# Optimization experiments

Measured on AMD Instinct MI355X. Metric: run time of the kernel, lower is better.

Reference implementation:

```python
import jax, jax.numpy as jnp
import numpy as np

N = 4096        # nodes == batch_size (GFN operates on dense N x N adjacency)
E = 65536       # edges per view (avg degree 16)
IN = 512        # per-view input feature dim
HV = [128, 64]  # per-view GCN dims
HM = [64, 64]   # fused-graph GCN dims
VIEWS = 3


def setup_inputs() -> dict:
    key = jax.random.key(0)
    ks = iter(jax.random.split(key, 64))

    def xavier(shape):
        lim = float(np.sqrt(6.0 / (shape[0] + shape[1])))
        return jax.random.uniform(next(ks), shape, minval=-lim, maxval=lim, dtype=jnp.float32)

    inp = {}
    for v in range(VIEWS):
        inp[f"x{v}"] = jax.random.normal(next(ks), (N, IN), dtype=jnp.float32)
        inp[f"src{v}"] = jax.random.randint(next(ks), (E,), 0, N, dtype=jnp.int32)
        inp[f"dst{v}"] = jax.random.randint(next(ks), (E,), 0, N, dtype=jnp.int32)
        inp[f"Wv{v}0"] = xavier((IN, HV[0]))
        inp[f"bv{v}0"] = jnp.zeros((HV[0],), jnp.float32)
        inp[f"Wv{v}1"] = xavier((HV[0], HV[1]))
        inp[f"bv{v}1"] = jnp.zeros((HV[1],), jnp.float32)
        inp[f"Wf{v}"] = xavier((HV[1], HV[1]))  # FeatureFusion weight
    # GFN: Linear(N -> N/2) -> ReLU -> Linear(N/2 -> N)
    inp["Wg1"] = xavier((N, N // 2)); inp["bg1"] = jnp.zeros((N // 2,), jnp.float32)
    inp["Wg2"] = xavier((N // 2, N)); inp["bg2"] = jnp.zeros((N,), jnp.float32)
    # fused-graph GCN layers
    inp["Wm0"] = xavier((HV[1], HM[0])); inp["bm0"] = jnp.zeros((HM[0],), jnp.float32)
    inp["Wm1"] = xavier((HM[0], HM[1])); inp["bm1"] = jnp.zeros((HM[1],), jnp.float32)
    return inp


def _deg_norms(src, dst):
    # DGL GraphConv norm='both': scale by out-deg(src)^-1/2 and in-deg(dst)^-1/2, degrees clamped to >=1
    ones = jnp.ones(src.shape[0], jnp.float32)
    dout = jnp.maximum(jax.ops.segment_sum(ones, src, num_segments=N), 1.0)
    din = jnp.maximum(jax.ops.segment_sum(ones, dst, num_segments=N), 1.0)
    return dout ** -0.5, din ** -0.5


def _gconv(x, W, b, src, dst, do_isqrt, di_isqrt, act):
    h = (x * do_isqrt[:, None]) @ W            # [N, out] (W commutes with row scaling)
    agg = jax.ops.segment_sum(h[src], dst, num_segments=N)
    h = agg * di_isqrt[:, None] + b
    return act(h)


def reference(x0, x1, x2, src0, dst0, src1, dst1, src2, dst2,
              Wv00, bv00, Wv01, bv01, Wv10, bv10, Wv11, bv11, Wv20, bv20, Wv21, bv21,
              Wf0, Wf1, Wf2, Wg1, bg1, Wg2, bg2, Wm0, bm0, Wm1, bm1):
    ident = lambda t: t
    xs = [x0, x1, x2]
    edges = [(src0, dst0), (src1, dst1), (src2, dst2)]
    Wv = [(Wv00, bv00, Wv01, bv01), (Wv10, bv10, Wv11, bv11), (Wv20, bv20, Wv21, bv21)]
    Wf = [Wf0, Wf1, Wf2]

    # per-view GCN stacks (relu on first layer, identity on last)
    feats = []
    for v in range(VIEWS):
        src, dst = edges[v]
        do_i, di_i = _deg_norms(src, dst)
        W0, b0, W1, b1 = Wv[v]
        f = _gconv(xs[v], W0, b0, src, dst, do_i, di_i, jax.nn.relu)
        f = _gconv(f, W1, b1, src, dst, do_i, di_i, ident)
        feats.append(f)

    # FeatureFusion (dropout omitted for determinism): sum(f @ Wf), softmax over features, relu
    z = feats[0] @ Wf[0] + feats[1] @ Wf[1] + feats[2] @ Wf[2]
    z = jax.nn.relu(jax.nn.softmax(z, axis=1))

    # consensus graph: sum of per-view dense adjacencies -> GFN -> clamp -> round(+0.1)
    adj = jnp.zeros((N, N), jnp.float32)
    for src, dst in edges:
        adj = adj + jnp.zeros((N, N), jnp.float32).at[src, dst].set(1.0)
    fused = jax.nn.relu(adj @ Wg1 + bg1) @ Wg2 + bg2
    fused = jnp.round(jnp.clip(fused, 0.0, 1.0) + 0.1)
    adj_r = fused

    # rebuild binary graph (went through numpy in original -> stop_gradient), symmetrize, add self-loops
    sym = jax.lax.stop_gradient(fused)
    sym = sym + sym.T
    A = jnp.maximum((sym > 0).astype(jnp.float32), jnp.eye(N, dtype=jnp.float32))
    deg = A.sum(axis=1)
    dn = deg ** -0.5

    # fused-graph GCN layers (dense normalized SpMM form since A is already dense)
    h = z
    h = jax.nn.relu(((A @ (h * dn[:, None])) * dn[:, None]) @ Wm0 + bm0)
    h = ((A @ (h * dn[:, None])) * dn[:, None]) @ Wm1 + bm1

    # InnerProductDecoder with identity activation; all `views` entries of adj_rec are identical
    adj_rec = h @ h.T
    return (adj_r, adj_rec, h)
```

## Files before the change

kernel.cpp:

```cpp
#include <hip/hip_runtime.h>
#include <math.h>

#define NNODES 4096
#define NEDGES 65536

typedef short bf16x8 __attribute__((ext_vector_type(8)));
typedef short short4v __attribute__((ext_vector_type(4)));
typedef float f32x4 __attribute__((ext_vector_type(4)));

struct Ptr3  { const float* p[3]; };
struct Ptr3i { const int*   p[3]; };
struct Ptr3h { const short* p[3]; };

__device__ __forceinline__ short f2bf(float f) {
    unsigned u = __builtin_bit_cast(unsigned, f);
    unsigned r = (u + 0x7FFFu + ((u >> 16) & 1u)) >> 16;
    return (short)r;
}
__device__ __forceinline__ float bf2f(short s) {
    return __builtin_bit_cast(float, ((unsigned)(unsigned short)s) << 16);
}

__device__ __forceinline__ void gload_lds16(const void* g, void* l) {
    __builtin_amdgcn_global_load_lds(
        (const __attribute__((address_space(1))) unsigned*)g,
        (__attribute__((address_space(3))) unsigned*)l, 16, 0, 0);
}

template<int ACT>
__global__ __launch_bounds__(512, 1)
void gm_k(const short* __restrict__ A, const short* __restrict__ Bt,
          const float* __restrict__ bias, void* __restrict__ Cout, void* __restrict__ Cout1,
          unsigned char* __restrict__ Pout, int M, int Nn, int K, int lda, int ldb)
{
    constexpr int SLOT = 32768;
    __shared__ short lds[2 * SLOT];
    const int tid = threadIdx.x;
    const int lane = tid & 63;
    const int wave = tid >> 6;
    const int wm = wave >> 2, wn = wave & 3;
    const int z = blockIdx.z;
    A  += (size_t)z * K;
    Bt += (size_t)z * K;
    void* Cw = (ACT == 3 && z == 1) ? Cout1 : Cout;
    const int gx = gridDim.x, nwg = gx * gridDim.y;
    int w = blockIdx.y * gx + blockIdx.x;
    const int q8 = nwg >> 3;
    w = (w & 7) * q8 + (w >> 3);
    const int bm0 = (w / gx) * 256, bn0 = (w % gx) * 256;
    const int NT = K >> 6;

    auto stageH = [&](int t, int part) {
        if (t >= NT) return;
        const int k0 = t << 6;
        char* base = (char*)(lds + (t & 1) * SLOT);
        const int isB = (part < 2);
        const int h = part & 1;
#pragma unroll
        for (int r = 0; r < 2; ++r) {
            int o = r * 8192 + tid * 16;
            int row = o >> 7;
            int grow = h * 128 + row;
            int scol = (((o >> 4) & 7) ^ (grow & 7)) << 3;
            const short* gsrc = isB ? (Bt + (size_t)(bn0 + grow) * ldb + k0 + scol)
                                    : (A  + (size_t)(bm0 + grow) * lda + k0 + scol);
            gload_lds16(gsrc, base + (isB ? 32768 : 0) + h * 16384 + r * 8192 + wave * 1024);
        }
    };

    f32x4 acc[8][4] = {};
    bf16x8 aF[4][2];
    bf16x8 bF[4][2];

#define PH(QM, QN, TCUR, T1, P1, T2, P2, VM)                                          \
    {                                                                                 \
        const short* As_ = lds + ((TCUR) & 1) * SLOT;                                 \
        const short* Bs_ = As_ + 16384;                                               \
        if constexpr ((QN) == 0) {                                                    \
            _Pragma("unroll") for (int kk = 0; kk < 2; ++kk) {                        \
                const int h_ = kk * 4 + (lane >> 4);                                  \
                _Pragma("unroll") for (int i = 0; i < 4; ++i) {                       \
                    int r_ = wm * 128 + (QM) * 64 + i * 16 + (lane & 15);             \
                    aF[i][kk] = *(const bf16x8*)(As_ + r_ * 64 + ((h_ ^ (r_ & 7)) << 3)); \
                }                                                                     \
            }                                                                         \
        }                                                                             \
        if constexpr ((QM) == 0) {                                                    \
            _Pragma("unroll") for (int kk = 0; kk < 2; ++kk) {                        \
                const int h_ = kk * 4 + (lane >> 4);                                  \
                _Pragma("unroll") for (int j = 0; j < 2; ++j) {                       \
                    int r_ = wn * 64 + ((QN) * 2 + j) * 16 + (lane & 15);             \
                    bF[(QN) * 2 + j][kk] = *(const bf16x8*)(Bs_ + r_ * 64 + ((h_ ^ (r_ & 7)) << 3)); \
                }                                                                     \
            }                                                                         \
        }                                                                             \
        if ((P1) >= 0) stageH(T1, P1);                                                \
        if ((P2) >= 0) stageH(T2, P2);                                                \
        if constexpr ((QM) == 0 && (QN) == 0) {                                       \
            asm volatile("s_waitcnt lgkmcnt(8)" ::: "memory");                        \
        }                                                                             \
        __builtin_amdgcn_s_barrier();                                                 \
        __builtin_amdgcn_s_setprio(1);                                                \
        _Pragma("unroll") for (int kk = 0; kk < 2; ++kk)                              \
            _Pragma("unroll") for (int i = 0; i < 4; ++i)                             \
                _Pragma("unroll") for (int j = 0; j < 2; ++j)                         \
                    acc[(QM) * 4 + i][(QN) * 2 + j] =                                 \
                        __builtin_amdgcn_mfma_f32_16x16x32_bf16(                      \
                            aF[i][kk], bF[(QN) * 2 + j][kk],                          \
                            acc[(QM) * 4 + i][(QN) * 2 + j], 0, 0, 0);                \
        __builtin_amdgcn_s_setprio(0);                                                \
        if ((VM) == 6)      { asm volatile("s_waitcnt vmcnt(6)" ::: "memory");        \
                              __builtin_amdgcn_sched_barrier(0); }                    \
        else if ((VM) == 0) { asm volatile("s_waitcnt vmcnt(0)" ::: "memory");        \
                              __builtin_amdgcn_sched_barrier(0); }                    \
        __builtin_amdgcn_s_barrier();                                                 \
    }

    stageH(0, 0); stageH(0, 1); stageH(0, 2); stageH(0, 3);
    if (NT > 1) { stageH(1, 0); stageH(1, 1); stageH(1, 2); }
    if (NT > 1) { asm volatile("s_waitcnt vmcnt(6)" ::: "memory"); }
    else        { asm volatile("s_waitcnt vmcnt(0)" ::: "memory"); }
    __builtin_amdgcn_sched_barrier(0);
    __builtin_amdgcn_s_barrier();

    for (int it = 0; it < NT / 2; ++it) {
        const int t0 = 2 * it, t1 = t0 + 1, t2 = t0 + 2, t3 = t0 + 3;
        const int vm4 = (t2 < NT) ? 6 : 0;
        const int vm8 = (t3 < NT) ? 6 : 0;
        PH(0, 0, t0, t1, 3,  0, -1, -1)
        PH(0, 1, t0,  0, -1, 0, -1, -1)
        PH(1, 0, t0, t2, 0, t2,  1, -1)
        PH(1, 1, t0, t2, 2,  0, -1, vm4)
        PH(0, 0, t1, t2, 3,  0, -1, -1)
        PH(0, 1, t1,  0, -1, 0, -1, -1)
        PH(1, 0, t1, t3, 0, t3,  1, -1)
        PH(1, 1, t1, t3, 2,  0, -1, vm8)
    }
    if (NT & 1) {
        const int tl = NT - 1;
        PH(0, 0, tl, 0, -1, 0, -1, -1)
        PH(0, 1, tl, 0, -1, 0, -1, -1)
        PH(1, 0, tl, 0, -1, 0, -1, -1)
        PH(1, 1, tl, 0, -1, 0, -1, -1)
    }
#undef PH

    const int cr = (lane >> 4) * 4;
    const int cc = lane & 15;
#pragma unroll
    for (int im = 0; im < 8; ++im) {
#pragma unroll
        for (int jn = 0; jn < 4; ++jn) {
            int col = bn0 + wn * 64 + jn * 16 + cc;
            float bv = bias ? bias[col] : 0.f;
#pragma unroll
            for (int q2 = 0; q2 < 4; ++q2) {
                int row = bm0 + wm * 128 + (im >> 2) * 64 + (im & 3) * 16 + cr + q2;
                float v = acc[im][jn][q2] + bv;
                if constexpr (ACT == 2) {
                    v = rintf(fminf(fmaxf(v, 0.f), 1.f) + 0.1f);
                    ((float*)Cw)[(size_t)row * Nn + col] = v;
                    Pout[(size_t)row * Nn + col] = (unsigned char)(v > 0.5f);
                } else if constexpr (ACT == 3) {
                    ((short*)Cw)[(size_t)row * Nn + col] = f2bf(v);
                } else {
                    ((float*)Cw)[(size_t)row * Nn + col] = v;
                }
            }
        }
    }
}

__global__ void reduce_h1_k(const short* __restrict__ p0, const short* __restrict__ p1,
                            const float* __restrict__ bias, short* __restrict__ H1b)
{
    int i = (blockIdx.x * 256 + threadIdx.x) * 8;
    bf16x8 a = *(const bf16x8*)(p0 + i);
    bf16x8 b = *(const bf16x8*)(p1 + i);
    int col = i & 2047;
    bf16x8 o;
#pragma unroll
    for (int j = 0; j < 8; ++j) {
        float v = bf2f(a[j]) + bf2f(b[j]) + bias[col + j];
        o[j] = f2bf(fmaxf(v, 0.f));
    }
    *(bf16x8*)(H1b + i) = o;
}

__global__ __launch_bounds__(256)
void mfma_gemm_b_k(const short* __restrict__ Aall, Ptr3h Btv, float* __restrict__ Call,
                   int M, int Nn, int K)
{
    __shared__ short As[64 * 64];
    __shared__ short Bs[64 * 64];
    const int z = blockIdx.z;
    const short* A = Aall + (size_t)z * M * K;
    const short* Bt = Btv.p[z];
    float* C = Call + (size_t)z * M * Nn;
    const int tid = threadIdx.x;
    const int lane = tid & 63, wave = tid >> 6;
    const int bm0 = blockIdx.y * 64, bn0 = blockIdx.x * 64;
    const int wr = (wave >> 1) * 32, wc = (wave & 1) * 32;

    f32x4 acc[2][2] = {};

    for (int k0 = 0; k0 < K; k0 += 64) {
        for (int c = wave; c < 8; c += 4) {
            int o = c * 1024 + lane * 16;
            int row = o >> 7;
            int sl = (o >> 4) & 7;
            int ss = sl ^ (row & 7);
            gload_lds16(A + ((size_t)(bm0 + row) * K + k0 + ss * 8), As + c * 512);
            gload_lds16(Bt + ((size_t)(bn0 + row) * K + k0 + ss * 8), Bs + c * 512);
        }
        __syncthreads();
#pragma unroll
        for (int kk = 0; kk < 2; ++kk) {
            bf16x8 a[2], b[2];
            const int khalf = kk * 4 + (lane >> 4);
#pragma unroll
            for (int i = 0; i < 2; ++i) {
                int r = wr + i * 16 + (lane & 15);
                a[i] = *(const bf16x8*)(As + r * 64 + ((khalf ^ (r & 7)) << 3));
            }
#pragma unroll
            for (int j = 0; j < 2; ++j) {
                int r = wc + j * 16 + (lane & 15);
                b[j] = *(const bf16x8*)(Bs + r * 64 + ((khalf ^ (r & 7)) << 3));
            }
#pragma unroll
            for (int i = 0; i < 2; ++i)
#pragma unroll
                for (int j = 0; j < 2; ++j)
                    acc[i][j] = __builtin_amdgcn_mfma_f32_16x16x32_bf16(a[i], b[j], acc[i][j], 0, 0, 0);
        }
        __syncthreads();
    }

    const int cr = (lane >> 4) * 4;
    const int cc = lane & 15;
#pragma unroll
    for (int i = 0; i < 2; ++i)
#pragma unroll
        for (int j = 0; j < 2; ++j)
#pragma unroll
            for (int q = 0; q < 4; ++q) {
                int row = bm0 + wr + i * 16 + cr + q;
                int col = bn0 + wc + j * 16 + cc;
                C[(size_t)row * Nn + col] = acc[i][j][q];
            }
}

__global__ __launch_bounds__(256)
void spmm_mfma_k(const short* __restrict__ A2b, const short* __restrict__ XsT,
                 float* __restrict__ part)
{
    __shared__ short As[64 * 64];
    __shared__ short Bs[128 * 64];
    const int tid = threadIdx.x;
    const int lane = tid & 63, wave = tid >> 6;
    const int kc = blockIdx.x, m0 = blockIdx.y * 64;
    const int wr = (wave >> 1) * 32, wc = (wave & 1) * 32;
    const int woff = wave * 512;

    f32x4 acc[2][2] = {};

    for (int k0 = kc * 512; k0 < kc * 512 + 512; k0 += 64) {
#pragma unroll
        for (int r = 0; r < 2; ++r) {
            int o = r * 4096 + tid * 16;
            int row = o >> 7;
            int sl = (o >> 4) & 7;
            gload_lds16(A2b + ((size_t)(m0 + row) * 4096 + k0 + ((sl ^ (row & 7)) << 3)),
                        As + r * 2048 + woff);
        }
#pragma unroll
        for (int r = 0; r < 4; ++r) {
            int o = r * 4096 + tid * 16;
            int row = o >> 7;
            int sl = (o >> 4) & 7;
            gload_lds16(XsT + ((size_t)row * 4096 + k0 + ((sl ^ (row & 7)) << 3)),
                        Bs + r * 2048 + woff);
        }
        __syncthreads();
#pragma unroll
        for (int kk = 0; kk < 2; ++kk) {
            const int h = kk * 4 + (lane >> 4);
            bf16x8 a[2], bh[2], bl[2];
#pragma unroll
            for (int i = 0; i < 2; ++i) {
                int r = wr + i * 16 + (lane & 15);
                a[i] = *(const bf16x8*)(As + r * 64 + ((h ^ (r & 7)) << 3));
            }
#pragma unroll
            for (int j = 0; j < 2; ++j) {
                int r = wc + j * 16 + (lane & 15);
                bh[j] = *(const bf16x8*)(Bs + r * 64 + ((h ^ (r & 7)) << 3));
                int r2 = r + 64;
                bl[j] = *(const bf16x8*)(Bs + r2 * 64 + ((h ^ (r2 & 7)) << 3));
            }
#pragma unroll
            for (int i = 0; i < 2; ++i)
#pragma unroll
                for (int j = 0; j < 2; ++j) {
                    acc[i][j] = __builtin_amdgcn_mfma_f32_16x16x32_bf16(a[i], bh[j], acc[i][j], 0, 0, 0);
                    acc[i][j] = __builtin_amdgcn_mfma_f32_16x16x32_bf16(a[i], bl[j], acc[i][j], 0, 0, 0);
                }
        }
        __syncthreads();
    }

    const int cr = (lane >> 4) * 4;
    const int cc = lane & 15;
#pragma unroll
    for (int i = 0; i < 2; ++i)
#pragma unroll
        for (int j = 0; j < 2; ++j)
#pragma unroll
            for (int q = 0; q < 4; ++q)
                part[((size_t)kc * NNODES + m0 + wr + i * 16 + cr + q) * 64 + wc + j * 16 + cc]
                    = acc[i][j][q];
}

__global__ void xsT_k(const float* __restrict__ X, const int* __restrict__ degA,
                      short* __restrict__ XsT)
{
    const int n = blockIdx.y;
    const int k = blockIdx.x * 256 + threadIdx.x;
    float v = X[(size_t)k * 64 + n] * (1.0f / sqrtf((float)degA[k]));
    short hi = f2bf(v);
    short lo = f2bf(v - bf2f(hi));
    XsT[(size_t)n * 4096 + k] = hi;
    XsT[(size_t)(64 + n) * 4096 + k] = lo;
}

__global__ void f32_to_bf16T_k(const float* __restrict__ src, short* __restrict__ dstT,
                               int R, int C)
{
    __shared__ float t[64][65];
    const int br = blockIdx.y * 64, bc = blockIdx.x * 64;
    for (int idx = threadIdx.x; idx < 64 * 64; idx += 256) {
        int r = idx >> 6, c = idx & 63;
        t[r][c] = src[(size_t)(br + r) * C + bc + c];
    }
    __syncthreads();
    for (int idx = threadIdx.x; idx < 64 * 64; idx += 256) {
        int c = idx >> 6, r = idx & 63;
        dstT[(size_t)(bc + c) * R + br + r] = f2bf(t[r][c]);
    }
}

__global__ void mask_to_bf16_k(const unsigned* __restrict__ mask, short* __restrict__ adj,
                               int words)
{
    int t = blockIdx.x * 256 + threadIdx.x;
    if (t < words) {
        unsigned w = mask[t];
        short4v o;
        o.x = f2bf((float)__popc(w & 0x7u));
        o.y = f2bf((float)__popc(w & 0x700u));
        o.z = f2bf((float)__popc(w & 0x70000u));
        o.w = f2bf((float)__popc(w & 0x7000000u));
        *(short4v*)(adj + (size_t)t * 4) = o;
    }
}

__global__ void xsplit_k(Ptr3 xv, const float* __restrict__ isq, short* __restrict__ xe)
{
    const int z = blockIdx.y;
    int t = blockIdx.x * 256 + threadIdx.x;
    int n = t >> 9, k = t & 511;
    float a = xv.p[z][(size_t)n * 512 + k] * isq[2 * z * NNODES + n];
    short hi = f2bf(a);
    short lo = f2bf(a - bf2f(hi));
    short* row = xe + (size_t)z * NNODES * 1536 + (size_t)n * 1536;
    row[k] = hi; row[512 + k] = hi; row[1024 + k] = lo;
}

__global__ void wsplitT_k(Ptr3 Wv, short* __restrict__ out, int K, int Nn)
{
    const int z = blockIdx.y;
    int t = blockIdx.x * 256 + threadIdx.x;
    if (t >= K * Nn) return;
    int k = t / Nn, n = t % Nn;
    float w = Wv.p[z][(size_t)k * Nn + n];
    short hi = f2bf(w);
    short lo = f2bf(w - bf2f(hi));
    short* row = out + (size_t)z * Nn * 3 * K + (size_t)n * 3 * K;
    row[k] = hi; row[K + k] = lo; row[2 * K + k] = hi;
}

template<int RELU>
__global__ __launch_bounds__(256)
void redgemm_k(const float* __restrict__ part, const int* __restrict__ degA,
               const float* __restrict__ Wm, const float* __restrict__ bias,
               float* __restrict__ out, short* __restrict__ Ae, short* __restrict__ Be,
               short* __restrict__ XsT)
{
    __shared__ float Ws[64 * 64];
    const int tid = threadIdx.x;
    for (int i = tid; i < 4096; i += 256) Ws[i] = Wm[i];
    __syncthreads();
    const int lane = tid & 63, wave = tid >> 6;
    const float bv = bias[lane];
    for (int rr = 0; rr < 4; ++rr) {
        int row = blockIdx.x * 16 + wave * 4 + rr;
        float s = 0.f;
#pragma unroll
        for (int p = 0; p < 8; ++p) s += part[((size_t)p * NNODES + row) * 64 + lane];
        const float dn = 1.0f / sqrtf((float)degA[row]);
        s *= dn;
        float acc = bv;
#pragma unroll
        for (int k = 0; k < 64; ++k)
            acc = fmaf(__shfl(s, k), Ws[k * 64 + lane], acc);
        if (RELU) acc = fmaxf(acc, 0.f);
        out[(size_t)row * 64 + lane] = acc;
        if (Ae) {
            short hi = f2bf(acc);
            short lo = f2bf(acc - bf2f(hi));
            size_t ro = (size_t)row * 192;
            Ae[ro + lane] = hi; Ae[ro + 64 + lane] = hi; Ae[ro + 128 + lane] = lo;
            Be[ro + lane] = hi; Be[ro + 64 + lane] = lo; Be[ro + 128 + lane] = hi;
        }
        if (XsT) {
            float vv = acc * dn;
            short hi = f2bf(vv);
            short lo = f2bf(vv - bf2f(hi));
            XsT[(size_t)lane * 4096 + row] = hi;
            XsT[(size_t)(64 + lane) * 4096 + row] = lo;
        }
    }
}

__global__ void edge_k(Ptr3i src, Ptr3i dst, unsigned* __restrict__ mask, int* __restrict__ degs)
{
    int e = blockIdx.x * 256 + threadIdx.x;
    int z = blockIdx.y;
    if (e < NEDGES) {
        int s = src.p[z][e], d = dst.p[z][e];
        unsigned c = (unsigned)s * (unsigned)NNODES + (unsigned)d;
        atomicOr(&mask[c >> 2], 1u << ((c & 3u) * 8u + (unsigned)z));
        atomicAdd(&degs[2 * z * NNODES + s], 1);
        atomicAdd(&degs[(2 * z + 1) * NNODES + d], 1);
    }
}

__global__ void deg_norm_k(const int* __restrict__ degs, float* __restrict__ isq, int n)
{
    int t = blockIdx.x * 256 + threadIdx.x;
    if (t < n) isq[t] = 1.0f / sqrtf(fmaxf((float)t >= 0 ? (float)degs[t] : 1.0f, 1.0f));
}

__global__ __launch_bounds__(1024)
void scan_k(const int* __restrict__ degs, int* __restrict__ rowptr, int* __restrict__ cursor)
{
    const int z = blockIdx.x;
    const int* din = degs + (2 * z + 1) * NNODES;
    __shared__ int sm[1024];
    const int t = threadIdx.x;
    int v0 = din[t * 4], v1 = din[t * 4 + 1], v2 = din[t * 4 + 2], v3 = din[t * 4 + 3];
    int c1 = v0 + v1, c2 = c1 + v2, s = c2 + v3;
    sm[t] = s;
    __syncthreads();
    for (int off = 1; off < 1024; off <<= 1) {
        int add = (t >= off) ? sm[t - off] : 0;
        __syncthreads();
        sm[t] += add;
        __syncthreads();
    }
    int base = sm[t] - s;
    int* rp = rowptr + z * NNODES;
    int* cu = cursor + z * NNODES;
    rp[t * 4] = base;          cu[t * 4] = base;
    rp[t * 4 + 1] = base + v0; cu[t * 4 + 1] = base + v0;
    rp[t * 4 + 2] = base + c1; cu[t * 4 + 2] = base + c1;
    rp[t * 4 + 3] = base + c2; cu[t * 4 + 3] = base + c2;
}

__global__ void fill_k(Ptr3i src, Ptr3i dst, int* __restrict__ cursor, int* __restrict__ eidx)
{
    int e = blockIdx.x * 256 + threadIdx.x;
    int z = blockIdx.y;
    if (e < NEDGES) {
        int d = dst.p[z][e];
        int pos = atomicAdd(&cursor[z * NNODES + d], 1);
        eidx[(size_t)z * NEDGES + pos] = src.p[z][e];
    }
}

template<int F, int ACT, int MODE>
__global__ void gather_k(const float* __restrict__ Hpre, const int* __restrict__ eidx,
                         const int* __restrict__ rowptr, const int* __restrict__ degs,
                         const float* __restrict__ isq, Ptr3 bias, short* __restrict__ Sout)
{
    const int z = blockIdx.y;
    const int tid = threadIdx.x;
    const int node = blockIdx.x * (256 / F) + tid / F;
    const int f = tid % F;
    const float* H = Hpre + (size_t)z * NNODES * F;
    const int base = rowptr[z * NNODES + node];
    const int cnt = degs[(2 * z + 1) * NNODES + node];
    const int* ei = eidx + (size_t)z * NEDGES + base;
    float s = 0.f;
    for (int i = 0; i < cnt; ++i) s += H[(size_t)ei[i] * F + f];
    float v = s * isq[(2 * z + 1) * NNODES + node] + bias.p[z][f];
    if (ACT) v = fmaxf(v, 0.f);
    if (MODE == 1) v *= isq[2 * z * NNODES + node];
    short hi = f2bf(v);
    short lo = f2bf(v - bf2f(hi));
    short* row = Sout + (size_t)z * NNODES * 3 * F + (size_t)node * 3 * F;
    row[f] = hi; row[F + f] = hi; row[2 * F + f] = lo;
}

__global__ void softsum_k(const float* __restrict__ zp, float* __restrict__ z)
{
    int row = blockIdx.x * 4 + (threadIdx.x >> 6);
    int f = threadIdx.x & 63;
    size_t i = (size_t)row * 64 + f;
    float v = zp[i] + zp[i + (size_t)NNODES * 64] + zp[i + (size_t)2 * NNODES * 64];
    float m = v;
#pragma unroll
    for (int off = 32; off >= 1; off >>= 1) m = fmaxf(m, __shfl_xor(m, off));
    float e = expf(v - m);
    float s = e;
#pragma unroll
    for (int off = 32; off >= 1; off >>= 1) s += __shfl_xor(s, off);
    z[i] = e / s;
}

__global__ __launch_bounds__(256)
void build_A2_k(const unsigned char* __restrict__ P, short* __restrict__ A2b,
                int* __restrict__ degA)
{
    __shared__ unsigned Ts[64][20];
    const int bi = blockIdx.y * 64, bj = blockIdx.x * 64;
    const int tid = threadIdx.x;
    const int r = tid >> 2, seg = tid & 3;
    uint4 tv = *(const uint4*)(P + (size_t)(bj + r) * NNODES + bi + seg * 16);
    Ts[r][seg * 4 + 0] = tv.x; Ts[r][seg * 4 + 1] = tv.y;
    Ts[r][seg * 4 + 2] = tv.z; Ts[r][seg * 4 + 3] = tv.w;
    __syncthreads();
    uint4 dv = *(const uint4*)(P + (size_t)(bi + r) * NNODES + bj + seg * 16);
    unsigned dw[4] = {dv.x, dv.y, dv.z, dv.w};
    const unsigned char* Tb = (const unsigned char*)Ts;
    bf16x8 o0, o1;
    int psum = 0;
#pragma unroll
    for (int w = 0; w < 4; ++w) {
#pragma unroll
        for (int b = 0; b < 4; ++b) {
            int idx = w * 4 + b;
            int j = seg * 16 + idx;
            unsigned a = (dw[w] >> (8 * b)) & 1u;
            unsigned tr = Tb[j * 80 + r] & 1u;
            unsigned on = a | tr | (unsigned)((bi + r) == (bj + j));
            short val = on ? (short)0x3F80 : (short)0;
            if (idx < 8) o0[idx] = val; else o1[idx - 8] = val;
            psum += (int)on;
        }
    }
    short* dst = A2b + (size_t)(bi + r) * NNODES + bj + seg * 16;
    *(bf16x8*)dst = o0;
    *(bf16x8*)(dst + 8) = o1;
    psum += __shfl_xor(psum, 1);
    psum += __shfl_xor(psum, 2);
    if (seg == 0) atomicAdd(&degA[bi + r], psum);
}

extern "C" void kernel_launch(void* const* d_in, const int* in_sizes, int n_in,
                              void* d_out, int out_size, void* d_ws, size_t ws_size,
                              hipStream_t stream)
{
    const int N = NNODES, E = NEDGES;
    const size_t MB = 1024 * 1024;

    const float* x[3]; const int* src[3]; const int* dst[3];
    const float *Wv0[3], *bv0[3], *Wv1[3], *bv1[3], *Wf[3];
    for (int v = 0; v < 3; ++v) {
        const int b = v * 8;
        x[v]   = (const float*)d_in[b + 0];
        src[v] = (const int*)  d_in[b + 1];
        dst[v] = (const int*)  d_in[b + 2];
        Wv0[v] = (const float*)d_in[b + 3];
        bv0[v] = (const float*)d_in[b + 4];
        Wv1[v] = (const float*)d_in[b + 5];
        bv1[v] = (const float*)d_in[b + 6];
        Wf[v]  = (const float*)d_in[b + 7];
    }
    const float* Wg1 = (const float*)d_in[24];
    const float* bg1 = (const float*)d_in[25];
    const float* Wg2 = (const float*)d_in[26];
    const float* bg2 = (const float*)d_in[27];
    const float* Wm0 = (const float*)d_in[28];
    const float* bm0 = (const float*)d_in[29];
    const float* Wm1 = (const float*)d_in[30];
    const float* bm1 = (const float*)d_in[31];

    float* out_adjr = (float*)d_out;
    float* out_rec  = out_adjr + (size_t)N * N;
    float* out_h    = out_rec + (size_t)N * N;

    char* oa = (char*)out_adjr;
    short* AdjB = (short*)oa;
    float* hv1  = (float*)(oa + 32 * MB);
    short* Ae2  = (short*)(oa + 38 * MB);
    short* Ae3  = (short*)(oa + 47 * MB);
    float* hv2  = (float*)(oa + 52 * MB);
    float* zp   = (float*)(oa + 56 * MB);
    short* partg0 = (short*)(oa + 32 * MB);
    short* partg1 = (short*)(oa + 48 * MB);

    char* orc = (char*)out_rec;
    short* xe   = (short*)orc;
    short* H1b  = (short*)orc;
    unsigned char* P = (unsigned char*)(orc + 16 * MB);
    short* Wg1T = (short*)(orc + 16 * MB);
    short* Wg2T = (short*)(orc + 32 * MB);
    float* part = (float*)(orc + 48 * MB);

    char* p = (char*)d_ws;
    unsigned* mask = (unsigned*)p;
    short* AeF = (short*)p;
    short* BeF = AeF + (size_t)N * 192;
    p += (size_t)N * N;
    int* degs = (int*)p;     p += (size_t)6 * N * 4;
    float* isq = (float*)p;  p += (size_t)6 * N * 4;
    int* rowptr = (int*)p;   p += (size_t)3 * N * 4;
    int* cursor = (int*)p;   p += (size_t)3 * N * 4;
    int* eidx = (int*)p;     p += (size_t)3 * E * 4;
    int* degA = (int*)p;     p += (size_t)N * 4;
    float* zbuf = (float*)p; p += (size_t)N * 64 * 4;
    float* h1m = (float*)p;  p += (size_t)N * 64 * 4;
    short* XsT = (short*)p;  p += (size_t)128 * N * 2;
    short* Wv0T = (short*)p; p += (size_t)3 * 128 * 1536 * 2;
    short* Wv1T = (short*)p; p += (size_t)3 * 64 * 384 * 2;
    short* WfT  = (short*)p; p += (size_t)3 * 64 * 192 * 2;
    short* A2b = (short*)((char*)d_ws + 64 * MB);

    Ptr3i srcP, dstP;
    for (int v = 0; v < 3; ++v) { srcP.p[v] = src[v]; dstP.p[v] = dst[v]; }

    hipMemsetAsync(mask, 0, (size_t)N * N, stream);
    hipMemsetAsync(degs, 0, (size_t)6 * N * 4, stream);

    edge_k<<<dim3((E + 255) / 256, 3), 256, 0, stream>>>(srcP, dstP, mask, degs);
    deg_norm_k<<<(6 * N + 255) / 256, 256, 0, stream>>>(degs, isq, 6 * N);
    scan_k<<<3, 1024, 0, stream>>>(degs, rowptr, cursor);
    fill_k<<<dim3((E + 255) / 256, 3), 256, 0, stream>>>(srcP, dstP, cursor, eidx);

    Ptr3 xP; for (int v = 0; v < 3; ++v) xP.p[v] = x[v];
    xsplit_k<<<dim3(N * 512 / 256, 3), 256, 0, stream>>>(xP, isq, xe);
    Ptr3 wP;
    for (int v = 0; v < 3; ++v) wP.p[v] = Wv0[v];
    wsplitT_k<<<dim3(512 * 128 / 256, 3), 256, 0, stream>>>(wP, Wv0T, 512, 128);
    for (int v = 0; v < 3; ++v) wP.p[v] = Wv1[v];
    wsplitT_k<<<dim3(128 * 64 / 256, 3), 256, 0, stream>>>(wP, Wv1T, 128, 64);
    for (int v = 0; v < 3; ++v) wP.p[v] = Wf[v];
    wsplitT_k<<<dim3(64 * 64 / 256, 3), 256, 0, stream>>>(wP, WfT, 64, 64);

    Ptr3h BtP; Ptr3 biasP;
    for (int v = 0; v < 3; ++v) BtP.p[v] = Wv0T + (size_t)v * 128 * 1536;
    mfma_gemm_b_k<<<dim3(2, N / 64, 3), 256, 0, stream>>>(xe, BtP, hv1, N, 128, 1536);
    for (int v = 0; v < 3; ++v) biasP.p[v] = bv0[v];
    gather_k<128, 1, 1><<<dim3(N / 2, 3), 256, 0, stream>>>(hv1, eidx, rowptr, degs, isq, biasP, Ae2);
    for (int v = 0; v < 3; ++v) BtP.p[v] = Wv1T + (size_t)v * 64 * 384;
    mfma_gemm_b_k<<<dim3(1, N / 64, 3), 256, 0, stream>>>(Ae2, BtP, hv2, N, 64, 384);
    for (int v = 0; v < 3; ++v) biasP.p[v] = bv1[v];
    gather_k<64, 0, 2><<<dim3(N / 4, 3), 256, 0, stream>>>(hv2, eidx, rowptr, degs, isq, biasP, Ae3);
    for (int v = 0; v < 3; ++v) BtP.p[v] = WfT + (size_t)v * 64 * 192;
    mfma_gemm_b_k<<<dim3(1, N / 64, 3), 256, 0, stream>>>(Ae3, BtP, zp, N, 64, 192);
    softsum_k<<<N / 4, 256, 0, stream>>>(zp, zbuf);

    mask_to_bf16_k<<<(N * N / 4 + 255) / 256, 256, 0, stream>>>(mask, AdjB, N * N / 4);
    f32_to_bf16T_k<<<dim3(2048 / 64, 4096 / 64), 256, 0, stream>>>(Wg1, Wg1T, 4096, 2048);
    f32_to_bf16T_k<<<dim3(4096 / 64, 2048 / 64), 256, 0, stream>>>(Wg2, Wg2T, 2048, 4096);

    gm_k<3><<<dim3(2048 / 256, 4096 / 256, 2), 512, 0, stream>>>(
        AdjB, Wg1T, nullptr, partg0, partg1, nullptr, 4096, 2048, 2048, 4096, 4096);
    reduce_h1_k<<<4096 * 2048 / 8 / 256, 256, 0, stream>>>(partg0, partg1, bg1, H1b);

    gm_k<2><<<dim3(4096 / 256, 4096 / 256, 1), 512, 0, stream>>>(
        H1b, Wg2T, bg2, out_adjr, nullptr, P, 4096, 4096, 2048, 2048, 2048);

    hipMemsetAsync(degA, 0, (size_t)N * 4, stream);
    build_A2_k<<<dim3(N / 64, N / 64), 256, 0, stream>>>(P, A2b, degA);

    xsT_k<<<dim3(16, 64), 256, 0, stream>>>(zbuf, degA, XsT);
    spmm_mfma_k<<<dim3(8, N / 64), 256, 0, stream>>>(A2b, XsT, part);
    redgemm_k<1><<<256, 256, 0, stream>>>(part, degA, Wm0, bm0, h1m, nullptr, nullptr, XsT);
    spmm_mfma_k<<<dim3(8, N / 64), 256, 0, stream>>>(A2b, XsT, part);
    redgemm_k<0><<<256, 256, 0, stream>>>(part, degA, Wm1, bm1, out_h, AeF, BeF, nullptr);

    gm_k<0><<<dim3(4096 / 256, 4096 / 256, 1), 512, 0, stream>>>(
        AeF, BeF, nullptr, out_rec, nullptr, nullptr, 4096, 4096, 192, 192, 192);
}
```

Before: 450.0 us.

## Fuse graph preprocessing and prep kernels, store fused adjacency as bytes

Merges the edge/degree/scan/fill kernels into a single per-view block that counts degrees in LDS, and removes a memset. It also packs the x/weight split kernels and the mask/Wg transposes into two multi-role launches. The symmetrized adjacency A2 is stored as uint8 instead of bf16 and expanded to bf16 inside the SpMM loader, halving its write and read traffic. The costs are a serialized 3-block graph kernel with heavy LDS atomics, and register-path loads in SpMM replacing the direct global-to-LDS loads.

```diff
diff --git a/kernel.cpp b/kernel.cpp
--- a/kernel.cpp
+++ b/kernel.cpp
@@ -187,6 +187,137 @@
     *(bf16x8*)(H1b + i) = o;
 }
 
+__global__ __launch_bounds__(1024)
+void graph_k(Ptr3i src, Ptr3i dst, unsigned* __restrict__ mask, int* __restrict__ dinG,
+             float* __restrict__ isq, int* __restrict__ rowptr, int* __restrict__ eidx)
+{
+    const int z = blockIdx.x;
+    __shared__ int dout[4096];
+    __shared__ int din[4096];
+    __shared__ int cur[4096];
+    __shared__ int sm[1024];
+    const int t = threadIdx.x;
+    for (int i = t; i < 4096; i += 1024) { dout[i] = 0; din[i] = 0; }
+    __syncthreads();
+    const int* sv = src.p[z];
+    const int* dv = dst.p[z];
+    for (int e = t; e < NEDGES; e += 1024) {
+        int s = sv[e], d = dv[e];
+        unsigned c = (unsigned)s * 4096u + (unsigned)d;
+        atomicOr(&mask[c >> 2], 1u << ((c & 3u) * 8u + (unsigned)z));
+        atomicAdd(&dout[s], 1);
+        atomicAdd(&din[d], 1);
+    }
+    __syncthreads();
+    for (int i = t; i < 4096; i += 1024) {
+        isq[2 * z * 4096 + i]       = 1.0f / sqrtf(fmaxf((float)dout[i], 1.0f));
+        isq[(2 * z + 1) * 4096 + i] = 1.0f / sqrtf(fmaxf((float)din[i], 1.0f));
+        dinG[z * 4096 + i] = din[i];
+    }
+    int v0 = din[t * 4], v1 = din[t * 4 + 1], v2 = din[t * 4 + 2], v3 = din[t * 4 + 3];
+    int c1 = v0 + v1, c2 = c1 + v2, s4 = c2 + v3;
+    sm[t] = s4;
+    __syncthreads();
+    for (int off = 1; off < 1024; off <<= 1) {
+        int add = (t >= off) ? sm[t - off] : 0;
+        __syncthreads();
+        sm[t] += add;
+        __syncthreads();
+    }
+    int base = sm[t] - s4;
+    cur[t * 4] = base;          cur[t * 4 + 1] = base + v0;
+    cur[t * 4 + 2] = base + c1; cur[t * 4 + 3] = base + c2;
+    int* rp = rowptr + z * 4096;
+    rp[t * 4] = base;          rp[t * 4 + 1] = base + v0;
+    rp[t * 4 + 2] = base + c1; rp[t * 4 + 3] = base + c2;
+    __syncthreads();
+    int* ei = eidx + (size_t)z * NEDGES;
+    for (int e = t; e < NEDGES; e += 1024) {
+        int pos = atomicAdd(&cur[dv[e]], 1);
+        ei[pos] = sv[e];
+    }
+}
+
+__device__ __forceinline__ void wsplit_body(const float* __restrict__ W, int K, int Nn,
+                                            short* __restrict__ out, int idx)
+{
+    int k = idx / Nn, n = idx % Nn;
+    float w = W[(size_t)k * Nn + n];
+    short hi = f2bf(w);
+    short lo = f2bf(w - bf2f(hi));
+    short* row = out + (size_t)n * 3 * K;
+    row[k] = hi; row[K + k] = lo; row[2 * K + k] = hi;
+}
+
+__global__ void prep_pv_k(Ptr3 xv, Ptr3 w0, Ptr3 w1, Ptr3 wf, const float* __restrict__ isq,
+                          short* __restrict__ xe, short* __restrict__ Wv0T,
+                          short* __restrict__ Wv1T, short* __restrict__ WfT)
+{
+    const int b = blockIdx.x;
+    const int tid = threadIdx.x;
+    if (b < 24576) {
+        int z = b / 8192;
+        int t = (b % 8192) * 256 + tid;
+        int n = t >> 9, k = t & 511;
+        float a = xv.p[z][(size_t)n * 512 + k] * isq[2 * z * NNODES + n];
+        short hi = f2bf(a);
+        short lo = f2bf(a - bf2f(hi));
+        short* row = xe + (size_t)z * NNODES * 1536 + (size_t)n * 1536;
+        row[k] = hi; row[512 + k] = hi; row[1024 + k] = lo;
+    } else if (b < 24576 + 768) {
+        int i = b - 24576;
+        int z = i / 256;
+        wsplit_body(w0.p[z], 512, 128, Wv0T + (size_t)z * 128 * 1536, (i % 256) * 256 + tid);
+    } else if (b < 24576 + 768 + 96) {
+        int i = b - 24576 - 768;
+        int z = i / 32;
+        wsplit_body(w1.p[z], 128, 64, Wv1T + (size_t)z * 64 * 384, (i % 32) * 256 + tid);
+    } else {
+        int i = b - 24576 - 768 - 96;
+        int z = i / 16;
+        wsplit_body(wf.p[z], 64, 64, WfT + (size_t)z * 64 * 192, (i % 16) * 256 + tid);
+    }
+}
+
+__global__ __launch_bounds__(256)
+void prep_gfn_k(const unsigned* __restrict__ mask, short* __restrict__ AdjB,
+                const float* __restrict__ Wg1, short* __restrict__ Wg1T,
+                const float* __restrict__ Wg2, short* __restrict__ Wg2T)
+{
+    __shared__ float tlds[64][65];
+    const int b = blockIdx.x;
+    const int tid = threadIdx.x;
+    if (b < 16384) {
+        int t = b * 256 + tid;
+        unsigned w = mask[t];
+        short4v o;
+        o.x = f2bf((float)__popc(w & 0x7u));
+        o.y = f2bf((float)__popc(w & 0x700u));
+        o.z = f2bf((float)__popc(w & 0x70000u));
+        o.w = f2bf((float)__popc(w & 0x7000000u));
+        *(short4v*)(AdjB + (size_t)t * 4) = o;
+        return;
+    }
+    const float* src; short* dstT; int R, C, bx, by;
+    if (b < 16384 + 2048) {
+        int i = b - 16384; bx = i % 32; by = i / 32;
+        src = Wg1; dstT = Wg1T; R = 4096; C = 2048;
+    } else {
+        int i = b - 16384 - 2048; bx = i % 64; by = i / 64;
+        src = Wg2; dstT = Wg2T; R = 2048; C = 4096;
+    }
+    const int br = by * 64, bc = bx * 64;
+    for (int idx = tid; idx < 64 * 64; idx += 256) {
+        int r = idx >> 6, c = idx & 63;
+        tlds[r][c] = src[(size_t)(br + r) * C + bc + c];
+    }
+    __syncthreads();
+    for (int idx = tid; idx < 64 * 64; idx += 256) {
+        int c = idx >> 6, r = idx & 63;
+        dstT[(size_t)(bc + c) * R + br + r] = f2bf(tlds[r][c]);
+    }
+}
+
 __global__ __launch_bounds__(256)
 void mfma_gemm_b_k(const short* __restrict__ Aall, Ptr3h Btv, float* __restrict__ Call,
                    int M, int Nn, int K)
@@ -252,7 +383,7 @@
 }
 
 __global__ __launch_bounds__(256)
-void spmm_mfma_k(const short* __restrict__ A2b, const short* __restrict__ XsT,
+void spmm_mfma_k(const unsigned char* __restrict__ A8, const short* __restrict__ XsT,
                  float* __restrict__ part)
 {
     __shared__ short As[64 * 64];
@@ -266,13 +397,20 @@
     f32x4 acc[2][2] = {};
 
     for (int k0 = kc * 512; k0 < kc * 512 + 512; k0 += 64) {
-#pragma unroll
-        for (int r = 0; r < 2; ++r) {
-            int o = r * 4096 + tid * 16;
-            int row = o >> 7;
-            int sl = (o >> 4) & 7;
-            gload_lds16(A2b + ((size_t)(m0 + row) * 4096 + k0 + ((sl ^ (row & 7)) << 3)),
-                        As + r * 2048 + woff);
+        {
+            int row = tid >> 2, cb = (tid & 3) * 16;
+            uint4 wv = *(const uint4*)(A8 + (size_t)(m0 + row) * 4096 + k0 + cb);
+            unsigned wa[4] = {wv.x, wv.y, wv.z, wv.w};
+            bf16x8 v0, v1;
+#pragma unroll
+            for (int bb = 0; bb < 8; ++bb)
+                v0[bb] = ((wa[bb >> 2] >> ((bb & 3) * 8)) & 0xFFu) ? (short)0x3F80 : (short)0;
+#pragma unroll
+            for (int bb = 0; bb < 8; ++bb)
+                v1[bb] = ((wa[2 + (bb >> 2)] >> ((bb & 3) * 8)) & 0xFFu) ? (short)0x3F80 : (short)0;
+            int s0 = (tid & 3) * 2;
+            *(bf16x8*)(As + row * 64 + ((s0 ^ (row & 7)) << 3)) = v0;
+            *(bf16x8*)(As + row * 64 + (((s0 + 1) ^ (row & 7)) << 3)) = v1;
         }
 #pragma unroll
         for (int r = 0; r < 4; ++r) {
@@ -332,62 +470,6 @@
     short lo = f2bf(v - bf2f(hi));
     XsT[(size_t)n * 4096 + k] = hi;
     XsT[(size_t)(64 + n) * 4096 + k] = lo;
-}
-
-__global__ void f32_to_bf16T_k(const float* __restrict__ src, short* __restrict__ dstT,
-                               int R, int C)
-{
-    __shared__ float t[64][65];
-    const int br = blockIdx.y * 64, bc = blockIdx.x * 64;
-    for (int idx = threadIdx.x; idx < 64 * 64; idx += 256) {
-        int r = idx >> 6, c = idx & 63;
-        t[r][c] = src[(size_t)(br + r) * C + bc + c];
-    }
-    __syncthreads();
-    for (int idx = threadIdx.x; idx < 64 * 64; idx += 256) {
-        int c = idx >> 6, r = idx & 63;
-        dstT[(size_t)(bc + c) * R + br + r] = f2bf(t[r][c]);
-    }
-}
-
-__global__ void mask_to_bf16_k(const unsigned* __restrict__ mask, short* __restrict__ adj,
-                               int words)
-{
-    int t = blockIdx.x * 256 + threadIdx.x;
-    if (t < words) {
-        unsigned w = mask[t];
-        short4v o;
-        o.x = f2bf((float)__popc(w & 0x7u));
-        o.y = f2bf((float)__popc(w & 0x700u));
-        o.z = f2bf((float)__popc(w & 0x70000u));
-        o.w = f2bf((float)__popc(w & 0x7000000u));
-        *(short4v*)(adj + (size_t)t * 4) = o;
-    }
-}
-
-__global__ void xsplit_k(Ptr3 xv, const float* __restrict__ isq, short* __restrict__ xe)
-{
-    const int z = blockIdx.y;
-    int t = blockIdx.x * 256 + threadIdx.x;
-    int n = t >> 9, k = t & 511;
-    float a = xv.p[z][(size_t)n * 512 + k] * isq[2 * z * NNODES + n];
-    short hi = f2bf(a);
-    short lo = f2bf(a - bf2f(hi));
-    short* row = xe + (size_t)z * NNODES * 1536 + (size_t)n * 1536;
-    row[k] = hi; row[512 + k] = hi; row[1024 + k] = lo;
-}
-
-__global__ void wsplitT_k(Ptr3 Wv, short* __restrict__ out, int K, int Nn)
-{
-    const int z = blockIdx.y;
-    int t = blockIdx.x * 256 + threadIdx.x;
-    if (t >= K * Nn) return;
-    int k = t / Nn, n = t % Nn;
-    float w = Wv.p[z][(size_t)k * Nn + n];
-    short hi = f2bf(w);
-    short lo = f2bf(w - bf2f(hi));
-    short* row = out + (size_t)z * Nn * 3 * K + (size_t)n * 3 * K;
-    row[k] = hi; row[K + k] = lo; row[2 * K + k] = hi;
 }
 
 template<int RELU>
@@ -433,65 +515,9 @@
     }
 }
 
-__global__ void edge_k(Ptr3i src, Ptr3i dst, unsigned* __restrict__ mask, int* __restrict__ degs)
-{
-    int e = blockIdx.x * 256 + threadIdx.x;
-    int z = blockIdx.y;
-    if (e < NEDGES) {
-        int s = src.p[z][e], d = dst.p[z][e];
-        unsigned c = (unsigned)s * (unsigned)NNODES + (unsigned)d;
-        atomicOr(&mask[c >> 2], 1u << ((c & 3u) * 8u + (unsigned)z));
-        atomicAdd(&degs[2 * z * NNODES + s], 1);
-        atomicAdd(&degs[(2 * z + 1) * NNODES + d], 1);
-    }
-}
-
-__global__ void deg_norm_k(const int* __restrict__ degs, float* __restrict__ isq, int n)
-{
-    int t = blockIdx.x * 256 + threadIdx.x;
-    if (t < n) isq[t] = 1.0f / sqrtf(fmaxf((float)t >= 0 ? (float)degs[t] : 1.0f, 1.0f));
-}
-
-__global__ __launch_bounds__(1024)
-void scan_k(const int* __restrict__ degs, int* __restrict__ rowptr, int* __restrict__ cursor)
-{
-    const int z = blockIdx.x;
-    const int* din = degs + (2 * z + 1) * NNODES;
-    __shared__ int sm[1024];
-    const int t = threadIdx.x;
-    int v0 = din[t * 4], v1 = din[t * 4 + 1], v2 = din[t * 4 + 2], v3 = din[t * 4 + 3];
-    int c1 = v0 + v1, c2 = c1 + v2, s = c2 + v3;
-    sm[t] = s;
-    __syncthreads();
-    for (int off = 1; off < 1024; off <<= 1) {
-        int add = (t >= off) ? sm[t - off] : 0;
-        __syncthreads();
-        sm[t] += add;
-        __syncthreads();
-    }
-    int base = sm[t] - s;
-    int* rp = rowptr + z * NNODES;
-    int* cu = cursor + z * NNODES;
-    rp[t * 4] = base;          cu[t * 4] = base;
-    rp[t * 4 + 1] = base + v0; cu[t * 4 + 1] = base + v0;
-    rp[t * 4 + 2] = base + c1; cu[t * 4 + 2] = base + c1;
-    rp[t * 4 + 3] = base + c2; cu[t * 4 + 3] = base + c2;
-}
-
-__global__ void fill_k(Ptr3i src, Ptr3i dst, int* __restrict__ cursor, int* __restrict__ eidx)
-{
-    int e = blockIdx.x * 256 + threadIdx.x;
-    int z = blockIdx.y;
-    if (e < NEDGES) {
-        int d = dst.p[z][e];
-        int pos = atomicAdd(&cursor[z * NNODES + d], 1);
-        eidx[(size_t)z * NEDGES + pos] = src.p[z][e];
-    }
-}
-
 template<int F, int ACT, int MODE>
 __global__ void gather_k(const float* __restrict__ Hpre, const int* __restrict__ eidx,
-                         const int* __restrict__ rowptr, const int* __restrict__ degs,
+                         const int* __restrict__ rowptr, const int* __restrict__ dinG,
                          const float* __restrict__ isq, Ptr3 bias, short* __restrict__ Sout)
 {
     const int z = blockIdx.y;
@@ -500,7 +526,7 @@
     const int f = tid % F;
     const float* H = Hpre + (size_t)z * NNODES * F;
     const int base = rowptr[z * NNODES + node];
-    const int cnt = degs[(2 * z + 1) * NNODES + node];
+    const int cnt = dinG[z * NNODES + node];
     const int* ei = eidx + (size_t)z * NEDGES + base;
     float s = 0.f;
     for (int i = 0; i < cnt; ++i) s += H[(size_t)ei[i] * F + f];
@@ -530,7 +556,7 @@
 }
 
 __global__ __launch_bounds__(256)
-void build_A2_k(const unsigned char* __restrict__ P, short* __restrict__ A2b,
+void build_A2_k(const unsigned char* __restrict__ P, unsigned char* __restrict__ A8,
                 int* __restrict__ degA)
 {
     __shared__ unsigned Ts[64][20];
@@ -544,25 +570,24 @@
     uint4 dv = *(const uint4*)(P + (size_t)(bi + r) * NNODES + bj + seg * 16);
     unsigned dw[4] = {dv.x, dv.y, dv.z, dv.w};
     const unsigned char* Tb = (const unsigned char*)Ts;
-    bf16x8 o0, o1;
+    unsigned ow[4];
     int psum = 0;
 #pragma unroll
     for (int w = 0; w < 4; ++w) {
+        unsigned o = 0;
 #pragma unroll
         for (int b = 0; b < 4; ++b) {
-            int idx = w * 4 + b;
-            int j = seg * 16 + idx;
+            int j = seg * 16 + w * 4 + b;
             unsigned a = (dw[w] >> (8 * b)) & 1u;
             unsigned tr = Tb[j * 80 + r] & 1u;
             unsigned on = a | tr | (unsigned)((bi + r) == (bj + j));
-            short val = on ? (short)0x3F80 : (short)0;
-            if (idx < 8) o0[idx] = val; else o1[idx - 8] = val;
+            o |= on << (8 * b);
             psum += (int)on;
         }
-    }
-    short* dst = A2b + (size_t)(bi + r) * NNODES + bj + seg * 16;
-    *(bf16x8*)dst = o0;
-    *(bf16x8*)(dst + 8) = o1;
+        ow[w] = o;
+    }
+    uint4 o4; o4.x = ow[0]; o4.y = ow[1]; o4.z = ow[2]; o4.w = ow[3];
+    *(uint4*)(A8 + (size_t)(bi + r) * NNODES + bj + seg * 16) = o4;
     psum += __shfl_xor(psum, 1);
     psum += __shfl_xor(psum, 2);
     if (seg == 0) atomicAdd(&degA[bi + r], psum);
@@ -615,8 +640,6 @@
     short* xe   = (short*)orc;
     short* H1b  = (short*)orc;
     unsigned char* P = (unsigned char*)(orc + 16 * MB);
-    short* Wg1T = (short*)(orc + 16 * MB);
-    short* Wg2T = (short*)(orc + 32 * MB);
     float* part = (float*)(orc + 48 * MB);
 
     char* p = (char*)d_ws;
@@ -624,10 +647,9 @@
     short* AeF = (short*)p;
     short* BeF = AeF + (size_t)N * 192;
     p += (size_t)N * N;
-    int* degs = (int*)p;     p += (size_t)6 * N * 4;
+    int* dinG = (int*)p;     p += (size_t)3 * N * 4;
     float* isq = (float*)p;  p += (size_t)6 * N * 4;
     int* rowptr = (int*)p;   p += (size_t)3 * N * 4;
-    int* cursor = (int*)p;   p += (size_t)3 * N * 4;
     int* eidx = (int*)p;     p += (size_t)3 * E * 4;
     int* degA = (int*)p;     p += (size_t)N * 4;
     float* zbuf = (float*)p; p += (size_t)N * 64 * 4;
@@ -636,46 +658,37 @@
     short* Wv0T = (short*)p; p += (size_t)3 * 128 * 1536 * 2;
     short* Wv1T = (short*)p; p += (size_t)3 * 64 * 384 * 2;
     short* WfT  = (short*)p; p += (size_t)3 * 64 * 192 * 2;
-    short* A2b = (short*)((char*)d_ws + 64 * MB);
+    unsigned char* A8 = (unsigned char*)d_ws + 64 * MB;
+    short* Wg1T = (short*)((char*)d_ws + 96 * MB);
+    short* Wg2T = (short*)((char*)d_ws + 112 * MB);
 
     Ptr3i srcP, dstP;
     for (int v = 0; v < 3; ++v) { srcP.p[v] = src[v]; dstP.p[v] = dst[v]; }
 
     hipMemsetAsync(mask, 0, (size_t)N * N, stream);
-    hipMemsetAsync(degs, 0, (size_t)6 * N * 4, stream);
-
-    edge_k<<<dim3((E + 255) / 256, 3), 256, 0, stream>>>(srcP, dstP, mask, degs);
-    deg_norm_k<<<(6 * N + 255) / 256, 256, 0, stream>>>(degs, isq, 6 * N);
-    scan_k<<<3, 1024, 0, stream>>>(degs, rowptr, cursor);
-    fill_k<<<dim3((E + 255) / 256, 3), 256, 0, stream>>>(srcP, dstP, cursor, eidx);
-
-    Ptr3 xP; for (int v = 0; v < 3; ++v) xP.p[v] = x[v];
-    xsplit_k<<<dim3(N * 512 / 256, 3), 256, 0, stream>>>(xP, isq, xe);
-    Ptr3 wP;
-    for (int v = 0; v < 3; ++v) wP.p[v] = Wv0[v];
-    wsplitT_k<<<dim3(512 * 128 / 256, 3), 256, 0, stream>>>(wP, Wv0T, 512, 128);
-    for (int v = 0; v < 3; ++v) wP.p[v] = Wv1[v];
-    wsplitT_k<<<dim3(128 * 64 / 256, 3), 256, 0, stream>>>(wP, Wv1T, 128, 64);
-    for (int v = 0; v < 3; ++v) wP.p[v] = Wf[v];
-    wsplitT_k<<<dim3(64 * 64 / 256, 3), 256, 0, stream>>>(wP, WfT, 64, 64);
+
+    graph_k<<<3, 1024, 0, stream>>>(srcP, dstP, mask, dinG, isq, rowptr, eidx);
+
+    prep_gfn_k<<<16384 + 2048 + 2048, 256, 0, stream>>>(mask, AdjB, Wg1, Wg1T, Wg2, Wg2T);
+
+    Ptr3 xP, w0P, w1P, wfP;
+    for (int v = 0; v < 3; ++v) { xP.p[v] = x[v]; w0P.p[v] = Wv0[v]; w1P.p[v] = Wv1[v]; wfP.p[v] = Wf[v]; }
+    prep_pv_k<<<24576 + 768 + 96 + 48, 256, 0, stream>>>(xP, w0P, w1P, wfP, isq,
+                                                          xe, Wv0T, Wv1T, WfT);
 
     Ptr3h BtP; Ptr3 biasP;
     for (int v = 0; v < 3; ++v) BtP.p[v] = Wv0T + (size_t)v * 128 * 1536;
     mfma_gemm_b_k<<<dim3(2, N / 64, 3), 256, 0, stream>>>(xe, BtP, hv1, N, 128, 1536);
     for (int v = 0; v < 3; ++v) biasP.p[v] = bv0[v];
-    gather_k<128, 1, 1><<<dim3(N / 2, 3), 256, 0, stream>>>(hv1, eidx, rowptr, degs, isq, biasP, Ae2);
+    gather_k<128, 1, 1><<<dim3(N / 2, 3), 256, 0, stream>>>(hv1, eidx, rowptr, dinG, isq, biasP, Ae2);
     for (int v = 0; v < 3; ++v) BtP.p[v] = Wv1T + (size_t)v * 64 * 384;
     mfma_gemm_b_k<<<dim3(1, N / 64, 3), 256, 0, stream>>>(Ae2, BtP, hv2, N, 64, 384);
     for (int v = 0; v < 3; ++v) biasP.p[v] = bv1[v];
-    gather_k<64, 0, 2><<<dim3(N / 4, 3), 256, 0, stream>>>(hv2, eidx, rowptr, degs, isq, biasP, Ae3);
+    gather_k<64, 0, 2><<<dim3(N / 4, 3), 256, 0, stream>>>(hv2, eidx, rowptr, dinG, isq, biasP, Ae3);
     for (int v = 0; v < 3; ++v) BtP.p[v] = WfT + (size_t)v * 64 * 192;
     mfma_gemm_b_k<<<dim3(1, N / 64, 3), 256, 0, stream>>>(Ae3, BtP, zp, N, 64, 192);
     softsum_k<<<N / 4, 256, 0, stream>>>(zp, zbuf);
 
-    mask_to_bf16_k<<<(N * N / 4 + 255) / 256, 256, 0, stream>>>(mask, AdjB, N * N / 4);
-    f32_to_bf16T_k<<<dim3(2048 / 64, 4096 / 64), 256, 0, stream>>>(Wg1, Wg1T, 4096, 2048);
-    f32_to_bf16T_k<<<dim3(4096 / 64, 2048 / 64), 256, 0, stream>>>(Wg2, Wg2T, 2048, 4096);
-
     gm_k<3><<<dim3(2048 / 256, 4096 / 256, 2), 512, 0, stream>>>(
         AdjB, Wg1T, nullptr, partg0, partg1, nullptr, 4096, 2048, 2048, 4096, 4096);
     reduce_h1_k<<<4096 * 2048 / 8 / 256, 256, 0, stream>>>(partg0, partg1, bg1, H1b);
@@ -684,12 +697,12 @@
         H1b, Wg2T, bg2, out_adjr, nullptr, P, 4096, 4096, 2048, 2048, 2048);
 
     hipMemsetAsync(degA, 0, (size_t)N * 4, stream);
-    build_A2_k<<<dim3(N / 64, N / 64), 256, 0, stream>>>(P, A2b, degA);
+    build_A2_k<<<dim3(N / 64, N / 64), 256, 0, stream>>>(P, A8, degA);
 
     xsT_k<<<dim3(16, 64), 256, 0, stream>>>(zbuf, degA, XsT);
-    spmm_mfma_k<<<dim3(8, N / 64), 256, 0, stream>>>(A2b, XsT, part);
+    spmm_mfma_k<<<dim3(8, N / 64), 256, 0, stream>>>(A8, XsT, part);
     redgemm_k<1><<<256, 256, 0, stream>>>(part, degA, Wm0, bm0, h1m, nullptr, nullptr, XsT);
-    spmm_mfma_k<<<dim3(8, N / 64), 256, 0, stream>>>(A2b, XsT, part);
+    spmm_mfma_k<<<dim3(8, N / 64), 256, 0, stream>>>(A8, XsT, part);
     redgemm_k<0><<<256, 256, 0, stream>>>(part, degA, Wm1, bm1, out_h, AeF, BeF, nullptr);
 
     gm_k<0><<<dim3(4096 / 256, 4096 / 256, 1), 512, 0, stream>>>(
```

Result: slower. 565.1 us (+25.6%).
